# Kernel optimization log

Measured on AMD Instinct MI355X. Metric: run time of the kernel, lower is better.

Reference implementation:

```python
import jax, jax.numpy as jnp
import numpy as np

N = 100_000   # nodes
E = 1_600_000 # edges
G = 512       # graphs in batch
DIN, DF, DOUT = 78, 32, 128
BN_EPS = 1e-5

def setup_inputs() -> dict:
    key = jax.random.key(0)
    ks = jax.random.split(key, 10)
    s = 0.1
    return {
        "x": jax.random.normal(ks[0], (N, DIN), jnp.float32),
        "edge_index": jax.random.randint(ks[1], (2, E), 0, N, dtype=jnp.int32),
        "batch": jnp.sort(jax.random.randint(ks[2], (N,), 0, G, dtype=jnp.int32)),
        "w1_in": jax.random.normal(ks[3], (DIN, DF), jnp.float32) * s,
        "b1_in": jnp.zeros((DF,), jnp.float32),
        "w1_out": jax.random.normal(ks[4], (DF, DF), jnp.float32) * s,
        "b1_out": jnp.zeros((DF,), jnp.float32),
        "wa": jax.random.normal(ks[5], (4, DF, DF), jnp.float32) * s,
        "ba": jnp.zeros((4, DF), jnp.float32),
        "wb": jax.random.normal(ks[6], (4, DF, DF), jnp.float32) * s,
        "bb": jnp.zeros((4, DF), jnp.float32),
        "gamma": jnp.ones((5, DF), jnp.float32),
        "beta": jnp.zeros((5, DF), jnp.float32),
        "fc_w": jax.random.normal(ks[7], (DF, DOUT), jnp.float32) * s,
        "fc_b": jnp.zeros((DOUT,), jnp.float32),
    }

def _gin_conv(h, src, dst, w1, bv1, w2, bv2):
    # GINConv with eps=0: nn(x + sum_{j in N(i)} x_j)
    agg = jax.ops.segment_sum(h[src], dst, num_segments=N)
    z = h + agg
    return jax.nn.relu(z @ w1 + bv1) @ w2 + bv2

def _bn(h, g, b):
    # BatchNorm1d, training-mode batch statistics (biased variance)
    mu = h.mean(axis=0)
    var = ((h - mu) ** 2).mean(axis=0)
    return g * (h - mu) * jax.lax.rsqrt(var + BN_EPS) + b

def reference(x, edge_index, batch, w1_in, b1_in, w1_out, b1_out,
              wa, ba, wb, bb, gamma, beta, fc_w, fc_b):
    src, dst = edge_index[0], edge_index[1]
    h = _bn(jax.nn.relu(_gin_conv(x, src, dst, w1_in, b1_in, w1_out, b1_out)), gamma[0], beta[0])
    for i in range(4):  # conv2..conv5 (identical shapes)
        h = _bn(jax.nn.relu(_gin_conv(h, src, dst, wa[i], ba[i], wb[i], bb[i])), gamma[i + 1], beta[i + 1])
    pooled = jax.ops.segment_sum(h, batch, num_segments=G)  # global_add_pool -> [G, DF]
    out = jax.nn.relu(pooled @ fc_w + fc_b)
    # dropout omitted (deterministic reference / eval semantics)
    return out
```

## Files before the change

kernel.cpp:

```cpp
#include <hip/hip_runtime.h>
#include <hip/hip_bf16.h>
#include <hip/hip_fp16.h>

#define NN 100000
#define EE 1600000
#define GG 512
#define DIN 78
#define DF 32
#define DOUT 128
#define BN_EPS 1e-5f

#define NBLK_NODE 3125

#define BSH 9
#define NBUCK 196
#define SCB 256
#define EPB (EE / SCB)

__device__ __forceinline__ unsigned short f2h(float f) {
    return __half_as_ushort(__float2half(f));
}
__device__ __forceinline__ float hlo(unsigned int v) {
    return __half2float(__ushort_as_half((unsigned short)(v & 0xFFFFu)));
}
__device__ __forceinline__ float hhi(unsigned int v) {
    return __half2float(__ushort_as_half((unsigned short)(v >> 16)));
}

__global__ __launch_bounds__(256) void k_bhist(const int* __restrict__ dst, int* __restrict__ hist_g) {
    __shared__ int hist[NBUCK];
    int tid = threadIdx.x, blk = blockIdx.x;
    if (tid < NBUCK) hist[tid] = 0;
    __syncthreads();
    int start = blk * EPB, end = start + EPB;
    for (int i = start + tid; i < end; i += 256) atomicAdd(&hist[dst[i] >> BSH], 1);
    __syncthreads();
    if (tid < NBUCK) hist_g[tid * SCB + blk] = hist[tid];
}

__global__ __launch_bounds__(256) void k_bscan(int* __restrict__ hist_g, int* __restrict__ bbase) {
    __shared__ int tot[256];
    int t = threadIdx.x;
    int total = 0;
    if (t < NBUCK)
        for (int blk = 0; blk < SCB; ++blk) total += hist_g[t * SCB + blk];
    tot[t] = (t < NBUCK) ? total : 0;
    __syncthreads();
    for (int off = 1; off < 256; off <<= 1) {
        int u = (t >= off) ? tot[t - off] : 0;
        __syncthreads();
        tot[t] += u;
        __syncthreads();
    }
    int excl = tot[t] - total;
    if (t < NBUCK) {
        bbase[t] = excl;
        int run = excl;
        for (int blk = 0; blk < SCB; ++blk) {
            int h = hist_g[t * SCB + blk];
            hist_g[t * SCB + blk] = run;
            run += h;
        }
    }
    if (t == 0) bbase[NBUCK] = EE;
}

__global__ __launch_bounds__(256) void k_bscatter(const int* __restrict__ src, const int* __restrict__ dst,
                                                  const int* __restrict__ hist_g, int* __restrict__ pairs) {
    __shared__ int base_l[NBUCK];
    __shared__ int cnt[NBUCK];
    int tid = threadIdx.x, blk = blockIdx.x;
    if (tid < NBUCK) { base_l[tid] = hist_g[tid * SCB + blk]; cnt[tid] = 0; }
    __syncthreads();
    int start = blk * EPB, end = start + EPB;
    for (int i = start + tid; i < end; i += 256) {
        int d = dst[i], s = src[i];
        int b = d >> BSH;
        int rk = atomicAdd(&cnt[b], 1);
        pairs[base_l[b] + rk] = s | ((d & 511) << 17);
    }
}

__global__ __launch_bounds__(256) void k_bfill(const int* __restrict__ pairs, const int* __restrict__ bbase,
                                               int* __restrict__ row_ptr, int* __restrict__ qoff,
                                               int* __restrict__ col) {
    __shared__ int c4[2048];
    __shared__ int nstart[512];
    __shared__ int ps[256];
    int tid = threadIdx.x, b = blockIdx.x;
    int base = bbase[b];
    int cntb = bbase[b + 1] - base;
    int nbase = b << BSH;
    int nloc = NN - nbase; if (nloc > 512) nloc = 512;
    for (int i = tid; i < 2048; i += 256) c4[i] = 0;
    __syncthreads();
    for (int i = tid; i < cntb; i += 256) {
        int v = pairs[base + i];
        int dloc = (unsigned)v >> 17;
        int q = (v & 0x1FFFF) >> 15;
        atomicAdd(&c4[dloc * 4 + q], 1);
    }
    __syncthreads();
    int n0 = 2 * tid, n1 = 2 * tid + 1;
    int t0 = c4[n0 * 4] + c4[n0 * 4 + 1] + c4[n0 * 4 + 2] + c4[n0 * 4 + 3];
    int t1 = c4[n1 * 4] + c4[n1 * 4 + 1] + c4[n1 * 4 + 2] + c4[n1 * 4 + 3];
    ps[tid] = t0 + t1;
    __syncthreads();
    for (int off = 1; off < 256; off <<= 1) {
        int u = (tid >= off) ? ps[tid - off] : 0;
        __syncthreads();
        ps[tid] += u;
        __syncthreads();
    }
    int pexcl = ps[tid] - (t0 + t1);
    nstart[n0] = pexcl;
    nstart[n1] = pexcl + t0;
    #pragma unroll
    for (int kk = 0; kk < 2; ++kk) {
        int n = (kk == 0) ? n0 : n1;
        if (n < nloc) {
            int s = nstart[n];
            int c0 = c4[n * 4], c1 = c4[n * 4 + 1], c2 = c4[n * 4 + 2];
            c4[n * 4]     = s;
            c4[n * 4 + 1] = s + c0;
            c4[n * 4 + 2] = s + c0 + c1;
            c4[n * 4 + 3] = s + c0 + c1 + c2;
            row_ptr[nbase + n] = base + s;
            qoff[nbase + n] = c0 | (c1 << 8) | (c2 << 16);
        }
    }
    if (b == 0 && tid == 0) row_ptr[NN] = EE;
    __syncthreads();
    for (int i = tid; i < cntb; i += 256) {
        int v = pairs[base + i];
        int dloc = (unsigned)v >> 17;
        int s = v & 0x1FFFF;
        int q = s >> 15;
        int lp = atomicAdd(&c4[dloc * 4 + q], 1);
        col[base + lp] = s;
    }
}

__global__ __launch_bounds__(256) void k_proj_first(const float* __restrict__ x,
                                                    const float* __restrict__ w1,
                                                    float* __restrict__ p,
                                                    unsigned short* __restrict__ pb) {
    __shared__ float w[DIN][DF];
    __shared__ float hx[32][DIN];
    int tid = threadIdx.x;
    for (int i = tid; i < DIN * DF; i += 256) w[i >> 5][i & 31] = w1[i];
    int base = blockIdx.x * 32;
    for (int i = tid; i < 32 * DIN; i += 256) hx[i / DIN][i % DIN] = x[base * DIN + i];
    __syncthreads();
    int j = tid & 31;
    #pragma unroll
    for (int it = 0; it < 4; ++it) {
        int rown = (tid >> 5) + 8 * it;
        float acc = 0.f;
        #pragma unroll
        for (int k = 0; k < DIN; ++k) acc += hx[rown][k] * w[k][j];
        p[(base + rown) * DF + j] = acc;
        pb[(base + rown) * DF + j] = f2h(acc);
    }
}

__global__ __launch_bounds__(256) void k_proj_hidden(const float* __restrict__ r,
                                                     const float* __restrict__ w1_,
                                                     const float* __restrict__ statsL,
                                                     const float* __restrict__ gamma,
                                                     const float* __restrict__ beta,
                                                     float* __restrict__ p,
                                                     unsigned short* __restrict__ pb) {
    __shared__ float w[DF][DF];
    __shared__ float h[32][DF + 1];
    int tid = threadIdx.x;
    for (int i = tid; i < DF * DF; i += 256) w[i >> 5][i & 31] = w1_[i];
    int grp = tid >> 3, c = tid & 7;
    int node = blockIdx.x * 32 + grp;
    const float invN = 1.0f / (float)NN;
    float4 s1v = ((const float4*)statsL)[c];
    float4 s2v = ((const float4*)(statsL + DF))[c];
    float4 gv  = ((const float4*)gamma)[c];
    float4 bv  = ((const float4*)beta)[c];
    float4 rv  = ((const float4*)r)[node * 8 + c];
    float mux = s1v.x * invN, muy = s1v.y * invN, muz = s1v.z * invN, muw = s1v.w * invN;
    float ivx = rsqrtf(s2v.x * invN - mux * mux + BN_EPS);
    float ivy = rsqrtf(s2v.y * invN - muy * muy + BN_EPS);
    float ivz = rsqrtf(s2v.z * invN - muz * muz + BN_EPS);
    float ivw = rsqrtf(s2v.w * invN - muw * muw + BN_EPS);
    h[grp][4 * c + 0] = gv.x * (rv.x - mux) * ivx + bv.x;
    h[grp][4 * c + 1] = gv.y * (rv.y - muy) * ivy + bv.y;
    h[grp][4 * c + 2] = gv.z * (rv.z - muz) * ivz + bv.z;
    h[grp][4 * c + 3] = gv.w * (rv.w - muw) * ivw + bv.w;
    __syncthreads();
    int j = tid & 31;
    #pragma unroll
    for (int it = 0; it < 4; ++it) {
        int rown = (tid >> 5) + 8 * it;
        float acc = 0.f;
        #pragma unroll
        for (int k = 0; k < DF; ++k) acc += h[rown][k] * w[k][j];
        p[(blockIdx.x * 32 + rown) * DF + j] = acc;
        pb[(blockIdx.x * 32 + rown) * DF + j] = f2h(acc);
    }
}

__global__ __launch_bounds__(256) void k_agg(const float* __restrict__ p,
                                             const unsigned short* __restrict__ pb,
                                             const int* __restrict__ row_ptr,
                                             const int* __restrict__ qoff,
                                             const int* __restrict__ col,
                                             const float* __restrict__ b1,
                                             const float* __restrict__ w2_,
                                             const float* __restrict__ b2,
                                             float* __restrict__ r,
                                             float* __restrict__ statsL) {
    __shared__ float w[DF][DF];
    __shared__ float a[32][DF + 1];
    __shared__ float red[4][2][DF];
    int tid = threadIdx.x;
    for (int i = tid; i < DF * DF; i += 256) w[i >> 5][i & 31] = w2_[i];
    int grp = tid >> 3, c = tid & 7;
    int base = blockIdx.x * 32;
    int node = base + grp;
    const float4* p4 = (const float4*)p;
    const uint2* pb2 = (const uint2*)pb;
    float4 b1v = ((const float4*)b1)[c];
    float4 self = p4[node * 8 + c];
    float4 acc0, acc1, acc2, acc3;
    acc0.x = self.x + b1v.x; acc0.y = self.y + b1v.y;
    acc0.z = self.z + b1v.z; acc0.w = self.w + b1v.w;
    acc1.x = acc1.y = acc1.z = acc1.w = 0.f;
    acc2.x = acc2.y = acc2.z = acc2.w = 0.f;
    acc3.x = acc3.y = acc3.z = acc3.w = 0.f;
    int e0 = row_ptr[node], e1 = row_ptr[node + 1];
    int qc = qoff[node];
    int q1 = e0 + (qc & 255);
    int q2 = q1 + ((qc >> 8) & 255);
    int q3 = q2 + ((qc >> 16) & 255);

    auto walk = [&](int s, int t) {
        int e = s;
        for (; e + 4 <= t; e += 4) {
            int s0 = col[e], s1 = col[e + 1], s2 = col[e + 2], s3 = col[e + 3];
            uint2 v0 = pb2[s0 * 8 + c];
            uint2 v1 = pb2[s1 * 8 + c];
            uint2 v2 = pb2[s2 * 8 + c];
            uint2 v3 = pb2[s3 * 8 + c];
            acc0.x += hlo(v0.x); acc0.y += hhi(v0.x); acc0.z += hlo(v0.y); acc0.w += hhi(v0.y);
            acc1.x += hlo(v1.x); acc1.y += hhi(v1.x); acc1.z += hlo(v1.y); acc1.w += hhi(v1.y);
            acc2.x += hlo(v2.x); acc2.y += hhi(v2.x); acc2.z += hlo(v2.y); acc2.w += hhi(v2.y);
            acc3.x += hlo(v3.x); acc3.y += hhi(v3.x); acc3.z += hlo(v3.y); acc3.w += hhi(v3.y);
        }
        for (; e < t; ++e) {
            uint2 v = pb2[col[e] * 8 + c];
            acc0.x += hlo(v.x); acc0.y += hhi(v.x); acc0.z += hlo(v.y); acc0.w += hhi(v.y);
        }
    };
    walk(e0, q1);
    __syncthreads();
    walk(q1, q2);
    __syncthreads();
    walk(q2, q3);
    __syncthreads();
    walk(q3, e1);

    acc0.x += acc1.x + acc2.x + acc3.x;
    acc0.y += acc1.y + acc2.y + acc3.y;
    acc0.z += acc1.z + acc2.z + acc3.z;
    acc0.w += acc1.w + acc2.w + acc3.w;
    a[grp][4 * c + 0] = fmaxf(acc0.x, 0.f);
    a[grp][4 * c + 1] = fmaxf(acc0.y, 0.f);
    a[grp][4 * c + 2] = fmaxf(acc0.z, 0.f);
    a[grp][4 * c + 3] = fmaxf(acc0.w, 0.f);
    __syncthreads();
    int j = tid & 31;
    float b2j = b2[j];
    float s1 = 0.f, s2 = 0.f;
    #pragma unroll
    for (int it = 0; it < 4; ++it) {
        int rown = (tid >> 5) + 8 * it;
        float accm = b2j;
        #pragma unroll
        for (int k = 0; k < DF; ++k) accm += a[rown][k] * w[k][j];
        float rv = fmaxf(accm, 0.f);
        r[(base + rown) * DF + j] = rv;
        s1 += rv;
        s2 += rv * rv;
    }
    s1 += __shfl_down(s1, 32);
    s2 += __shfl_down(s2, 32);
    int wave = tid >> 6, lane = tid & 63;
    if (lane < 32) { red[wave][0][j] = s1; red[wave][1][j] = s2; }
    __syncthreads();
    if (tid < 32) {
        float t1 = red[0][0][j] + red[1][0][j] + red[2][0][j] + red[3][0][j];
        float t2 = red[0][1][j] + red[1][1][j] + red[2][1][j] + red[3][1][j];
        atomicAdd(&statsL[j], t1);
        atomicAdd(&statsL[DF + j], t2);
    }
}

__global__ __launch_bounds__(256) void k_pool(const float* __restrict__ r,
                                              const float* __restrict__ statsL,
                                              const float* __restrict__ gamma,
                                              const float* __restrict__ beta,
                                              const int* __restrict__ batch,
                                              float* __restrict__ pooled) {
    int t = blockIdx.x * 256 + threadIdx.x;
    int nodeBase = (t >> 5) * 8;
    if (nodeBase >= NN) return;
    int j = t & 31;
    const float invN = 1.0f / (float)NN;
    float mu = statsL[j] * invN;
    float inv = rsqrtf(statsL[DF + j] * invN - mu * mu + BN_EPS);
    float gj = gamma[j], bj = beta[j];
    float accp = 0.f;
    int curg = batch[nodeBase];
    #pragma unroll
    for (int k = 0; k < 8; ++k) {
        int n = nodeBase + k;
        int g = batch[n];
        float val = gj * (r[n * DF + j] - mu) * inv + bj;
        if (g != curg) { atomicAdd(&pooled[curg * DF + j], accp); accp = 0.f; curg = g; }
        accp += val;
    }
    atomicAdd(&pooled[curg * DF + j], accp);
}

__global__ __launch_bounds__(128) void k_fc(const float* __restrict__ pooled,
                                            const float* __restrict__ fc_w,
                                            const float* __restrict__ fc_b,
                                            float* __restrict__ out) {
    __shared__ float pl[DF];
    int g = blockIdx.x, j = threadIdx.x;
    if (j < DF) pl[j] = pooled[g * DF + j];
    __syncthreads();
    float acc = fc_b[j];
    #pragma unroll
    for (int k = 0; k < DF; ++k) acc += pl[k] * fc_w[k * DOUT + j];
    out[g * DOUT + j] = fmaxf(acc, 0.f);
}

extern "C" void kernel_launch(void* const* d_in, const int* in_sizes, int n_in,
                              void* d_out, int out_size, void* d_ws, size_t ws_size,
                              hipStream_t stream) {
    const float* x      = (const float*)d_in[0];
    const int*   eidx   = (const int*)d_in[1];
    const int*   batch  = (const int*)d_in[2];
    const float* w1_in  = (const float*)d_in[3];
    const float* b1_in  = (const float*)d_in[4];
    const float* w1_out = (const float*)d_in[5];
    const float* b1_out = (const float*)d_in[6];
    const float* wa     = (const float*)d_in[7];
    const float* ba     = (const float*)d_in[8];
    const float* wb     = (const float*)d_in[9];
    const float* bb     = (const float*)d_in[10];
    const float* gamma  = (const float*)d_in[11];
    const float* beta   = (const float*)d_in[12];
    const float* fc_w   = (const float*)d_in[13];
    const float* fc_b   = (const float*)d_in[14];
    float* out = (float*)d_out;

    const int* esrc = eidx;
    const int* edst = eidx + EE;

    float* W = (float*)d_ws;
    float* p       = W;
    float* r       = p + (size_t)NN * DF;
    float* pooled  = r + (size_t)NN * DF;
    float* stats   = pooled + (size_t)GG * DF;
    int* row_ptr = (int*)(stats + 5 * 64);
    int* col     = row_ptr + (NN + 1);
    int* hist_g  = col + EE;
    int* bbase   = hist_g + NBUCK * SCB;
    unsigned short* pb = (unsigned short*)(bbase + NBUCK + 1);
    int* qoff    = (int*)(pb + (size_t)NN * DF);
    int* pairs   = (int*)p;

    k_bhist<<<SCB, 256, 0, stream>>>(edst, hist_g);
    k_bscan<<<1, 256, 0, stream>>>(hist_g, bbase);
    k_bscatter<<<SCB, 256, 0, stream>>>(esrc, edst, hist_g, pairs);
    k_bfill<<<NBUCK, 256, 0, stream>>>(pairs, bbase, row_ptr, qoff, col);

    hipMemsetAsync(stats, 0, sizeof(float) * 5 * 64, stream);

    k_proj_first<<<NBLK_NODE, 256, 0, stream>>>(x, w1_in, p, pb);
    k_agg<<<NBLK_NODE, 256, 0, stream>>>(p, pb, row_ptr, qoff, col, b1_in, w1_out, b1_out, r, stats);

    for (int i = 1; i < 5; ++i) {
        const float* w1_ = wa + (size_t)(i - 1) * DF * DF;
        const float* b1_ = ba + (size_t)(i - 1) * DF;
        const float* w2_ = wb + (size_t)(i - 1) * DF * DF;
        const float* b2_ = bb + (size_t)(i - 1) * DF;
        const float* g_  = gamma + (size_t)(i - 1) * DF;
        const float* be_ = beta + (size_t)(i - 1) * DF;
        k_proj_hidden<<<NBLK_NODE, 256, 0, stream>>>(r, w1_, stats + (i - 1) * 64, g_, be_, p, pb);
        k_agg<<<NBLK_NODE, 256, 0, stream>>>(p, pb, row_ptr, qoff, col, b1_, w2_, b2_, r, stats + i * 64);
    }

    hipMemsetAsync(pooled, 0, sizeof(float) * GG * DF, stream);
    k_pool<<<((NN / 8) * 32 + 255) / 256, 256, 0, stream>>>(r, stats + 4 * 64, gamma + 4 * DF,
                                                            beta + 4 * DF, batch, pooled);
    k_fc<<<GG, 128, 0, stream>>>(pooled, fc_w, fc_b, out);
}
```

Baseline: 822.6 us.

## Parallelize bucket scan across blocks and halve source-range partitions in aggregation

The single-block serial bucket scan is split into a per-bucket parallel scan kernel (one block per bucket) plus a small scan over bucket totals, with the scatter adding the bucket base. Separately, each node's edge list is now split into two source-index halves instead of four quarter ranges, which reduces the block-wide barriers in the aggregation kernel from three to one and simplifies the qoff encoding. The scan change targets a latency-bound single-block kernel in the CSR build. Using fewer source partitions loosens the lockstep ordering of gathers across the block, which may lower cache locality on the feature reads.

```diff
diff --git a/kernel.cpp b/kernel.cpp
--- a/kernel.cpp
+++ b/kernel.cpp
@@ -11,6 +11,7 @@
 #define BN_EPS 1e-5f
 
 #define NBLK_NODE 3125
+#define HALF_N 50000
 
 #define BSH 9
 #define NBUCK 196
@@ -38,39 +39,45 @@
     if (tid < NBUCK) hist_g[tid * SCB + blk] = hist[tid];
 }
 
-__global__ __launch_bounds__(256) void k_bscan(int* __restrict__ hist_g, int* __restrict__ bbase) {
-    __shared__ int tot[256];
+__global__ __launch_bounds__(256) void k_bscanA(int* __restrict__ hist_g, int* __restrict__ bbase) {
+    __shared__ int s[256];
+    int t = threadIdx.x, b = blockIdx.x;
+    int v = hist_g[b * SCB + t];
+    s[t] = v;
+    __syncthreads();
+    for (int off = 1; off < 256; off <<= 1) {
+        int u = (t >= off) ? s[t - off] : 0;
+        __syncthreads();
+        s[t] += u;
+        __syncthreads();
+    }
+    hist_g[b * SCB + t] = s[t] - v;
+    if (t == 255) bbase[b] = s[t];
+}
+
+__global__ __launch_bounds__(256) void k_bscanB(int* __restrict__ bbase) {
+    __shared__ int s[256];
     int t = threadIdx.x;
-    int total = 0;
-    if (t < NBUCK)
-        for (int blk = 0; blk < SCB; ++blk) total += hist_g[t * SCB + blk];
-    tot[t] = (t < NBUCK) ? total : 0;
+    int v = (t < NBUCK) ? bbase[t] : 0;
+    s[t] = v;
     __syncthreads();
     for (int off = 1; off < 256; off <<= 1) {
-        int u = (t >= off) ? tot[t - off] : 0;
-        __syncthreads();
-        tot[t] += u;
-        __syncthreads();
-    }
-    int excl = tot[t] - total;
-    if (t < NBUCK) {
-        bbase[t] = excl;
-        int run = excl;
-        for (int blk = 0; blk < SCB; ++blk) {
-            int h = hist_g[t * SCB + blk];
-            hist_g[t * SCB + blk] = run;
-            run += h;
-        }
-    }
+        int u = (t >= off) ? s[t - off] : 0;
+        __syncthreads();
+        s[t] += u;
+        __syncthreads();
+    }
+    if (t < NBUCK) bbase[t] = s[t] - v;
     if (t == 0) bbase[NBUCK] = EE;
 }
 
 __global__ __launch_bounds__(256) void k_bscatter(const int* __restrict__ src, const int* __restrict__ dst,
-                                                  const int* __restrict__ hist_g, int* __restrict__ pairs) {
+                                                  const int* __restrict__ hist_g, const int* __restrict__ bbase,
+                                                  int* __restrict__ pairs) {
     __shared__ int base_l[NBUCK];
     __shared__ int cnt[NBUCK];
     int tid = threadIdx.x, blk = blockIdx.x;
-    if (tid < NBUCK) { base_l[tid] = hist_g[tid * SCB + blk]; cnt[tid] = 0; }
+    if (tid < NBUCK) { base_l[tid] = bbase[tid] + hist_g[tid * SCB + blk]; cnt[tid] = 0; }
     __syncthreads();
     int start = blk * EPB, end = start + EPB;
     for (int i = start + tid; i < end; i += 256) {
@@ -84,7 +91,7 @@
 __global__ __launch_bounds__(256) void k_bfill(const int* __restrict__ pairs, const int* __restrict__ bbase,
                                                int* __restrict__ row_ptr, int* __restrict__ qoff,
                                                int* __restrict__ col) {
-    __shared__ int c4[2048];
+    __shared__ int c2[1024];
     __shared__ int nstart[512];
     __shared__ int ps[256];
     int tid = threadIdx.x, b = blockIdx.x;
@@ -92,18 +99,18 @@
     int cntb = bbase[b + 1] - base;
     int nbase = b << BSH;
     int nloc = NN - nbase; if (nloc > 512) nloc = 512;
-    for (int i = tid; i < 2048; i += 256) c4[i] = 0;
+    for (int i = tid; i < 1024; i += 256) c2[i] = 0;
     __syncthreads();
     for (int i = tid; i < cntb; i += 256) {
         int v = pairs[base + i];
         int dloc = (unsigned)v >> 17;
-        int q = (v & 0x1FFFF) >> 15;
-        atomicAdd(&c4[dloc * 4 + q], 1);
+        int q = ((v & 0x1FFFF) >= HALF_N) ? 1 : 0;
+        atomicAdd(&c2[dloc * 2 + q], 1);
     }
     __syncthreads();
     int n0 = 2 * tid, n1 = 2 * tid + 1;
-    int t0 = c4[n0 * 4] + c4[n0 * 4 + 1] + c4[n0 * 4 + 2] + c4[n0 * 4 + 3];
-    int t1 = c4[n1 * 4] + c4[n1 * 4 + 1] + c4[n1 * 4 + 2] + c4[n1 * 4 + 3];
+    int t0 = c2[n0 * 2] + c2[n0 * 2 + 1];
+    int t1 = c2[n1 * 2] + c2[n1 * 2 + 1];
     ps[tid] = t0 + t1;
     __syncthreads();
     for (int off = 1; off < 256; off <<= 1) {
@@ -120,13 +127,11 @@
         int n = (kk == 0) ? n0 : n1;
         if (n < nloc) {
             int s = nstart[n];
-            int c0 = c4[n * 4], c1 = c4[n * 4 + 1], c2 = c4[n * 4 + 2];
-            c4[n * 4]     = s;
-            c4[n * 4 + 1] = s + c0;
-            c4[n * 4 + 2] = s + c0 + c1;
-            c4[n * 4 + 3] = s + c0 + c1 + c2;
+            int c0 = c2[n * 2];
+            c2[n * 2]     = s;
+            c2[n * 2 + 1] = s + c0;
             row_ptr[nbase + n] = base + s;
-            qoff[nbase + n] = c0 | (c1 << 8) | (c2 << 16);
+            qoff[nbase + n] = c0;
         }
     }
     if (b == 0 && tid == 0) row_ptr[NN] = EE;
@@ -135,8 +140,8 @@
         int v = pairs[base + i];
         int dloc = (unsigned)v >> 17;
         int s = v & 0x1FFFF;
-        int q = s >> 15;
-        int lp = atomicAdd(&c4[dloc * 4 + q], 1);
+        int q = (s >= HALF_N) ? 1 : 0;
+        int lp = atomicAdd(&c2[dloc * 2 + q], 1);
         col[base + lp] = s;
     }
 }
@@ -234,10 +239,7 @@
     acc2.x = acc2.y = acc2.z = acc2.w = 0.f;
     acc3.x = acc3.y = acc3.z = acc3.w = 0.f;
     int e0 = row_ptr[node], e1 = row_ptr[node + 1];
-    int qc = qoff[node];
-    int q1 = e0 + (qc & 255);
-    int q2 = q1 + ((qc >> 8) & 255);
-    int q3 = q2 + ((qc >> 16) & 255);
+    int q1 = e0 + qoff[node];
 
     auto walk = [&](int s, int t) {
         int e = s;
@@ -259,11 +261,7 @@
     };
     walk(e0, q1);
     __syncthreads();
-    walk(q1, q2);
-    __syncthreads();
-    walk(q2, q3);
-    __syncthreads();
-    walk(q3, e1);
+    walk(q1, e1);
 
     acc0.x += acc1.x + acc2.x + acc3.x;
     acc0.y += acc1.y + acc2.y + acc3.y;
@@ -379,8 +377,9 @@
     int* pairs   = (int*)p;
 
     k_bhist<<<SCB, 256, 0, stream>>>(edst, hist_g);
-    k_bscan<<<1, 256, 0, stream>>>(hist_g, bbase);
-    k_bscatter<<<SCB, 256, 0, stream>>>(esrc, edst, hist_g, pairs);
+    k_bscanA<<<NBUCK, 256, 0, stream>>>(hist_g, bbase);
+    k_bscanB<<<1, 256, 0, stream>>>(bbase);
+    k_bscatter<<<SCB, 256, 0, stream>>>(esrc, edst, hist_g, bbase, pairs);
     k_bfill<<<NBUCK, 256, 0, stream>>>(pairs, bbase, row_ptr, qoff, col);
 
     hipMemsetAsync(stats, 0, sizeof(float) * 5 * 64, stream);
```

Measured after the change: 773.5 us. -6.0%, faster.
